# Kernel optimization log

Hardware: AMD Instinct MI355X
Metric: run time of the kernel (lower is better)

Reference implementation:

```python
import jax, jax.numpy as jnp
import numpy as np

DIM = 256
NUM_HEADS = 4
HEAD_DIM = DIM // NUM_HEADS


def _linear_params(k, d_in, d_out):
    kw, kb = jax.random.split(k)
    lim = 1.0 / np.sqrt(d_in)
    W = jax.random.uniform(kw, (d_out, d_in), jnp.float32, -lim, lim)
    b = jax.random.uniform(kb, (d_out,), jnp.float32, -lim, lim)
    return W, b


def setup_inputs() -> dict:
    key = jax.random.key(0)
    ks = jax.random.split(key, 10)
    B, Nq, Nkv = 8, 4096, 256
    inp = {
        'node_emb': jax.random.normal(ks[0], (B, Nq, DIM), jnp.float32),
        'cluster_emb': jax.random.normal(ks[1], (B, Nkv, DIM), jnp.float32),
        'clustering_weights': jax.random.normal(ks[2], (B, Nq, Nkv), jnp.float32),
        'ln_q_g': jnp.ones((DIM,), jnp.float32), 'ln_q_b': jnp.zeros((DIM,), jnp.float32),
        'ln_kv_g': jnp.ones((DIM,), jnp.float32), 'ln_kv_b': jnp.zeros((DIM,), jnp.float32),
        'ln_out_g': jnp.ones((DIM,), jnp.float32), 'ln_out_b': jnp.zeros((DIM,), jnp.float32),
    }
    for name, k in [('q', ks[3]), ('k', ks[4]), ('v', ks[5]), ('o', ks[6])]:
        W, b = _linear_params(k, DIM, DIM)
        inp[f'W_{name}'], inp[f'b_{name}'] = W, b
    W1, b1 = _linear_params(ks[7], DIM, DIM)
    W2, b2 = _linear_params(ks[8], DIM, DIM)
    inp.update(W_m1=W1, b_m1=b1, W_m2=W2, b_m2=b2)
    return inp


def _layer_norm(x, g, b, eps=1e-5):
    mu = jnp.mean(x, axis=-1, keepdims=True)
    var = jnp.var(x, axis=-1, keepdims=True)
    return (x - mu) * jax.lax.rsqrt(var + eps) * g + b


def reference(node_emb, cluster_emb, clustering_weights,
              ln_q_g, ln_q_b, ln_kv_g, ln_kv_b, ln_out_g, ln_out_b,
              W_q, b_q, W_k, b_k, W_v, b_v, W_o, b_o,
              W_m1, b_m1, W_m2, b_m2):
    B, Nq, D = node_emb.shape
    Nkv = cluster_emb.shape[1]
    q_in = _layer_norm(node_emb, ln_q_g, ln_q_b)
    kv_in = _layer_norm(cluster_emb, ln_kv_g, ln_kv_b)
    # projections -> [B, H, N, hd]
    Q = (q_in @ W_q.T + b_q).reshape(B, Nq, NUM_HEADS, HEAD_DIM).transpose(0, 2, 1, 3)
    K = (kv_in @ W_k.T + b_k).reshape(B, Nkv, NUM_HEADS, HEAD_DIM).transpose(0, 2, 1, 3)
    V = (kv_in @ W_v.T + b_v).reshape(B, Nkv, NUM_HEADS, HEAD_DIM).transpose(0, 2, 1, 3)
    scores = jnp.einsum('bhqd,bhkd->bhqk', Q, K) / np.sqrt(HEAD_DIM)
    scores = scores + clustering_weights[:, None, :, :]
    attn = jax.nn.softmax(scores, axis=-1)
    ctx = jnp.einsum('bhqk,bhkd->bhqd', attn, V)
    ctx = ctx.transpose(0, 2, 1, 3).reshape(B, Nq, D)
    attn_out = ctx @ W_o.T + b_o
    x = node_emb + attn_out
    h = _layer_norm(x, ln_out_g, ln_out_b)
    h = jax.nn.gelu(h @ W_m1.T + b_m1, approximate=False) @ W_m2.T + b_m2
    out = x + h
    attn_matrix = attn.mean(axis=1)
    return out, attn_matrix
```

## Files before the change

kernel.cpp:

```cpp
#include <hip/hip_runtime.h>
#include <math.h>

typedef __attribute__((ext_vector_type(8))) short short8;
typedef __attribute__((ext_vector_type(4))) float f32x4;
typedef __attribute__((ext_vector_type(2))) unsigned int u32x2;

#define AS1 __attribute__((address_space(1)))
#define AS3 __attribute__((address_space(3)))

__device__ __forceinline__ float b2f(short s){
  return __uint_as_float(((unsigned int)(unsigned short)s) << 16);
}
__device__ __forceinline__ short f2b(float f){
  unsigned int u = __float_as_uint(f);
  u = (u + 0x7fffu + ((u >> 16) & 1u)) >> 16;
  return (short)u;
}
__device__ __forceinline__ unsigned pk2(float lo, float hi){
  return ((unsigned)(unsigned short)f2b(hi) << 16) | (unsigned)(unsigned short)f2b(lo);
}
__device__ __forceinline__ float ulo(unsigned u){ return __uint_as_float(u << 16); }
__device__ __forceinline__ float uhi(unsigned u){ return __uint_as_float(u & 0xffff0000u); }

__global__ __launch_bounds__(256) void cvt_w(
    const float* __restrict__ s0, const float* __restrict__ s1,
    const float* __restrict__ s2, const float* __restrict__ s3,
    const float* __restrict__ s4, const float* __restrict__ s5,
    short* __restrict__ dst, short* __restrict__ dstS)
{
  const float* srcs[6] = {s0, s1, s2, s3, s4, s5};
  int i = blockIdx.x * 256 + threadIdx.x;
  int mat = i >> 16, rc = i & 65535;
  short v = f2b(srcs[mat][rc]);
  dst[i] = v;
  if (mat >= 3){
    int row = rc >> 8, col = rc & 255;
    int d2 = (mat - 3) * 65536 + ((col >> 5) << 13) + (row << 5)
           + (((col >> 3) & 3) << 3) + (col & 7);
    dstS[d2] = v;
  }
}

__global__ __launch_bounds__(256) void ln_k(
    const float* __restrict__ x, const float* __restrict__ g,
    const float* __restrict__ bta, short* __restrict__ y)
{
  const int row = blockIdx.x, t = threadIdx.x;
  const size_t base = (size_t)row * 256;
  float v = x[base + t];
  float s1 = v, s2 = v * v;
  #pragma unroll
  for (int off = 32; off; off >>= 1){ s1 += __shfl_down(s1, off); s2 += __shfl_down(s2, off); }
  __shared__ float a1[4], a2[4];
  __shared__ float mu_s, rs_s;
  if ((t & 63) == 0){ a1[t >> 6] = s1; a2[t >> 6] = s2; }
  __syncthreads();
  if (t == 0){
    float S1 = a1[0] + a1[1] + a1[2] + a1[3];
    float S2 = a2[0] + a2[1] + a2[2] + a2[3];
    float mu = S1 * 0.00390625f;
    float var = S2 * 0.00390625f - mu * mu;
    mu_s = mu; rs_s = rsqrtf(var + 1e-5f);
  }
  __syncthreads();
  y[base + t] = f2b((v - mu_s) * rs_s * g[t] + bta[t]);
}

template<int OT, int LNA>
__global__ __launch_bounds__(256, 2) void gemmW(
    const short* __restrict__ A, const float* __restrict__ Af,
    const short* __restrict__ W, const float* __restrict__ bias,
    short* __restrict__ outB,
    const float* __restrict__ lnag, const float* __restrict__ lnab)
{
  __shared__ short As[64][264];
  __shared__ short Ws[2][256][40];
  const int tid = threadIdx.x;
  const int m0 = blockIdx.x << 6;
  const int w = tid >> 6, lane = tid & 63;
  const int l15 = lane & 15, g = lane >> 4;

  if (LNA){
    const int row = tid >> 2, c0 = (tid & 3) << 6;
    float vv[64];
    const float* src = &Af[(size_t)(m0 + row) * 256 + c0];
    #pragma unroll
    for (int i = 0; i < 16; ++i) *(f32x4*)&vv[4 * i] = *(const f32x4*)&src[4 * i];
    float s1 = 0.f, s2 = 0.f;
    #pragma unroll
    for (int i = 0; i < 64; ++i){ s1 += vv[i]; s2 += vv[i] * vv[i]; }
    s1 += __shfl_xor(s1, 1); s2 += __shfl_xor(s2, 1);
    s1 += __shfl_xor(s1, 2); s2 += __shfl_xor(s2, 2);
    const float mu = s1 * 0.00390625f;
    const float rs = rsqrtf(s2 * 0.00390625f - mu * mu + 1e-5f);
    #pragma unroll
    for (int i = 0; i < 8; ++i){
      f32x4 gv0 = *(const f32x4*)&lnag[c0 + 8 * i];
      f32x4 gv1 = *(const f32x4*)&lnag[c0 + 8 * i + 4];
      f32x4 bv0 = *(const f32x4*)&lnab[c0 + 8 * i];
      f32x4 bv1 = *(const f32x4*)&lnab[c0 + 8 * i + 4];
      short8 o;
      #pragma unroll
      for (int j = 0; j < 4; ++j) o[j] = f2b((vv[8 * i + j] - mu) * rs * gv0[j] + bv0[j]);
      #pragma unroll
      for (int j = 0; j < 4; ++j) o[4 + j] = f2b((vv[8 * i + 4 + j] - mu) * rs * gv1[j] + bv1[j]);
      *(short8*)&As[row][c0 + 8 * i] = o;
    }
  } else {
    #pragma unroll
    for (int it = 0; it < 8; ++it){
      int idx = tid + (it << 8);
      int row = idx >> 5, c = (idx & 31) << 3;
      *(short8*)&As[row][c] = *(const short8*)&A[(size_t)(m0 + row) * 256 + c];
    }
  }
  #pragma unroll
  for (int it = 0; it < 4; ++it){
    int row = (it << 6) + (tid >> 2), c = (tid & 3) << 3;
    *(short8*)&Ws[0][row][c] = *(const short8*)&W[(size_t)row * 256 + c];
  }
  __syncthreads();

  f32x4 acc[16];
  #pragma unroll
  for (int nt = 0; nt < 16; ++nt) acc[nt] = {0.f, 0.f, 0.f, 0.f};

  int cur = 0;
  for (int s = 0; s < 8; ++s){
    const int k0 = s << 5;
    short8 wreg[4];
    if (s < 7){
      #pragma unroll
      for (int it = 0; it < 4; ++it)
        wreg[it] = *(const short8*)&W[(size_t)((it << 6) + (tid >> 2)) * 256 + k0 + 32 + ((tid & 3) << 3)];
    }
    short8 af = *(const short8*)&As[(w << 4) + l15][k0 + (g << 3)];
    #pragma unroll
    for (int nt = 0; nt < 16; ++nt){
      short8 bf = *(const short8*)&Ws[cur][(nt << 4) + l15][g << 3];
      acc[nt] = __builtin_amdgcn_mfma_f32_16x16x32_bf16(af, bf, acc[nt], 0, 0, 0);
    }
    if (s < 7){
      #pragma unroll
      for (int it = 0; it < 4; ++it)
        *(short8*)&Ws[cur ^ 1][(it << 6) + (tid >> 2)][(tid & 3) << 3] = wreg[it];
    }
    __syncthreads();
    cur ^= 1;
  }

  const int row_l = (w << 4) + (g << 2);
  #pragma unroll
  for (int nt = 0; nt < 16; ++nt){
    const int col = (nt << 4) + l15;
    const float bv = bias[col];
    #pragma unroll
    for (int r = 0; r < 4; ++r){
      const int m = m0 + row_l + r;
      float v = acc[nt][r] + bv;
      if (OT == 1){
        const int b_ = m >> 8, kvr = m & 255;
        const int knt = kvr >> 4, kl = kvr & 15;
        const int h = col >> 6, half = (col >> 5) & 1, kg = (col >> 3) & 3, kj = col & 7;
        outB[(((((size_t)(b_ * 4 + h) * 16 + knt) * 2 + half) * 4 + kg) * 16 + kl) * 8 + kj] = f2b(v);
      }
      if (OT == 2){
        const int b_ = m >> 8, kvj = m & 255;
        const int jp = (kvj & ~31) | (((kvj >> 2) & 3) << 3) | (((kvj >> 4) & 1) << 2) | (kvj & 3);
        const int h = col >> 6, dp = col & 63;
        const int kk = jp >> 5, vg = (jp >> 3) & 3, vj = jp & 7;
        const int vn2 = dp >> 4, vl = dp & 15;
        outB[(((((size_t)(b_ * 4 + h) * 8 + kk) * 4 + vn2) * 4 + vg) * 16 + vl) * 8 + vj] = f2b(v);
      }
      if (OT == 4){
        outB[((((size_t)blockIdx.x * 8 + (col >> 5)) * 4 + w) * 64
              + (((col >> 3) & 3) << 4) + (g << 2) + r) * 8 + (col & 7)] = f2b(v);
      }
    }
  }
}

__global__ __launch_bounds__(256, 2) void attn_k(
    const short* __restrict__ Qf, const short* __restrict__ Kf,
    const short* __restrict__ Vf, const float* __restrict__ cw,
    short* __restrict__ ctx, float* __restrict__ am_out)
{
  extern __shared__ __align__(16) short smem[];
  short* Kl = smem;
  short* Vl = smem + 16384;
  const int b = blockIdx.y;
  const int q0 = blockIdx.x << 6;
  const int tid = threadIdx.x;
  const int w = tid >> 6, lane = tid & 63;
  const int l15 = lane & 15, g = lane >> 4;
  const size_t qw = (size_t)b * 4096 + q0 + (w << 4);
  const size_t qblk = qw >> 4;
  const size_t tileQ = qblk >> 2;
  const int wQ = (int)(qblk & 3);
  const size_t tileC = (size_t)b * 64 + blockIdx.x;

#define STG(dst_, src_) do{ _Pragma("unroll")                                        \
  for (int it_ = 0; it_ < 8; ++it_){ int c_ = (it_ << 8) + tid;                      \
    __builtin_amdgcn_global_load_lds((const AS1 void*)((src_) + (c_ << 3)),          \
                                     (AS3 void*)((dst_) + (c_ << 3)), 16, 0, 0); } }while(0)

  unsigned cwp[16][2];
  f32x4 am[16];
  {
    char* reg = (char*)smem + (w << 13);
    #pragma unroll
    for (int j = 0; j < 16; ++j){
      f32x4 v = *(const f32x4*)&cw[(qw + j) * 256 + (lane << 2)];
      u32x2 d = { pk2(v[0], v[1]), pk2(v[2], v[3]) };
      unsigned off = ((j << 9) + (lane << 3)) ^ ((j & 7) << 4);
      *(u32x2*)(reg + off) = d;
    }
    __syncthreads();
    #pragma unroll
    for (int nt = 0; nt < 16; ++nt){
      unsigned base = ((l15 << 9) + (nt << 5) + (g << 3)) ^ ((l15 & 7) << 4);
      cwp[nt][0] = *(const unsigned*)(reg + base);
      cwp[nt][1] = *(const unsigned*)(reg + base + 4);
      am[nt] = {0.f, 0.f, 0.f, 0.f};
    }
    __syncthreads();
  }

  STG(Kl, Kf + ((size_t)(b * 4) << 14));
  __syncthreads();

  for (int h = 0; h < 4; ++h){
    STG(Vl, Vf + ((size_t)(b * 4 + h) << 14));
    short8 qf0 = *(const short8*)&Qf[(((tileQ * 8 + (h << 1)) * 4 + wQ) * 64 + lane) * 8];
    short8 qf1 = *(const short8*)&Qf[(((tileQ * 8 + (h << 1) + 1) * 4 + wQ) * 64 + lane) * 8];

    f32x4 acc[16];
    #pragma unroll
    for (int nt = 0; nt < 16; ++nt) acc[nt] = {0.f, 0.f, 0.f, 0.f};
    #pragma unroll
    for (int nt = 0; nt < 16; ++nt){
      short8 kf0 = *(const short8*)&Kl[(nt << 10) + (lane << 3)];
      acc[nt] = __builtin_amdgcn_mfma_f32_16x16x32_bf16(kf0, qf0, acc[nt], 0, 0, 0);
      short8 kf1 = *(const short8*)&Kl[(nt << 10) + 512 + (lane << 3)];
      acc[nt] = __builtin_amdgcn_mfma_f32_16x16x32_bf16(kf1, qf1, acc[nt], 0, 0, 0);
    }
    __syncthreads();
    if (h < 3) STG(Kl, Kf + ((size_t)(b * 4 + h + 1) << 14));

    float mx = -3.4e38f;
    #pragma unroll
    for (int nt = 0; nt < 16; ++nt){
      float c0 = __uint_as_float(cwp[nt][0] << 16);
      float c1 = __uint_as_float(cwp[nt][0] & 0xffff0000u);
      float c2 = __uint_as_float(cwp[nt][1] << 16);
      float c3 = __uint_as_float(cwp[nt][1] & 0xffff0000u);
      acc[nt][0] = acc[nt][0] * 0.125f + c0;
      acc[nt][1] = acc[nt][1] * 0.125f + c1;
      acc[nt][2] = acc[nt][2] * 0.125f + c2;
      acc[nt][3] = acc[nt][3] * 0.125f + c3;
      mx = fmaxf(mx, fmaxf(fmaxf(acc[nt][0], acc[nt][1]), fmaxf(acc[nt][2], acc[nt][3])));
    }
    mx = fmaxf(mx, __shfl_xor(mx, 16));
    mx = fmaxf(mx, __shfl_xor(mx, 32));
    float sm = 0.f;
    #pragma unroll
    for (int nt = 0; nt < 16; ++nt){
      #pragma unroll
      for (int r = 0; r < 4; ++r){
        float e = __expf(acc[nt][r] - mx);
        acc[nt][r] = e; sm += e;
      }
    }
    sm += __shfl_xor(sm, 16);
    sm += __shfl_xor(sm, 32);
    float inv = 1.f / sm;
    #pragma unroll
    for (int nt = 0; nt < 16; ++nt){
      #pragma unroll
      for (int r = 0; r < 4; ++r){
        float p = acc[nt][r] * inv;
        acc[nt][r] = p;
        am[nt][r] += 0.25f * p;
      }
    }
    f32x4 oc[4] = {{0,0,0,0},{0,0,0,0},{0,0,0,0},{0,0,0,0}};
    #pragma unroll
    for (int kk = 0; kk < 8; ++kk){
      union { short8 s; unsigned u[4]; } pa;
      pa.u[0] = pk2(acc[2 * kk][0],     acc[2 * kk][1]);
      pa.u[1] = pk2(acc[2 * kk][2],     acc[2 * kk][3]);
      pa.u[2] = pk2(acc[2 * kk + 1][0], acc[2 * kk + 1][1]);
      pa.u[3] = pk2(acc[2 * kk + 1][2], acc[2 * kk + 1][3]);
      #pragma unroll
      for (int n2 = 0; n2 < 4; ++n2){
        short8 vb = *(const short8*)&Vl[(((kk << 2) + n2) << 9) + (lane << 3)];
        oc[n2] = __builtin_amdgcn_mfma_f32_16x16x32_bf16(pa.s, vb, oc[n2], 0, 0, 0);
      }
    }
    #pragma unroll
    for (int n2 = 0; n2 < 4; ++n2){
      const int sctx = (h << 1) + (n2 >> 1);
      const int gctx = ((n2 & 1) << 1) + (l15 >> 3);
      const int j = l15 & 7;
      #pragma unroll
      for (int r = 0; r < 4; ++r)
        ctx[(((tileC * 8 + sctx) * 4 + w) * 64 + (gctx << 4) + (g << 2) + r) * 8 + j]
            = f2b(oc[n2][r]);
    }
    __syncthreads();
  }

  {
    char* reg = (char*)smem + (w << 14);
    #pragma unroll
    for (int nt = 0; nt < 16; ++nt){
      unsigned off = ((l15 << 10) + (nt << 6) + (g << 4)) ^ ((l15 & 7) << 4);
      *(f32x4*)(reg + off) = am[nt];
    }
    __syncthreads();
    #pragma unroll
    for (int i2 = 0; i2 < 16; ++i2){
      unsigned fb = (tid << 4) + (i2 << 12);
      unsigned rowin = (fb >> 10) & 15;
      f32x4 v = *(const f32x4*)((char*)smem + (fb ^ ((rowin & 7) << 4)));
      unsigned row = fb >> 10;
      *(f32x4*)&am_out[((size_t)b * 4096 + q0 + row) * 256 + ((fb & 1023) >> 2)] = v;
    }
  }
#undef STG
}

__global__ __launch_bounds__(256, 2) void tail_k(
    const short* __restrict__ ctxaf, const short* __restrict__ Wst,
    const float* __restrict__ b_o, const float* __restrict__ b_m1,
    const float* __restrict__ b_m2, const float* __restrict__ node,
    const float* __restrict__ lng, const float* __restrict__ lnb,
    float* __restrict__ outF)
{
  extern __shared__ __align__(16) short lds[];
  short* Ws0 = lds + 16896;
  short* Ws1 = Ws0 + 8192;
  const int tid = threadIdx.x;
  const int tile = blockIdx.x;
  const int m0 = tile << 6;
  const int w = tid >> 6, lane = tid & 63;
  const int l15 = lane & 15, g = lane >> 4;
  const int row_l = (w << 4) + (g << 2);

#define ASW(row_, col_) (*(short*)((char*)lds + (row_) * 528 + \
    (((col_) ^ ((((row_) >> 2) & 3) << 3)) << 1)))
#define ASR8(row_, boff_) (*(const short8*)((char*)lds + (row_) * 528 + \
    ((boff_) ^ ((((row_) >> 2) & 3) << 4))))
#define STGW(dst_, wmat_, s_) do{ _Pragma("unroll")                                  \
  for (int it_ = 0; it_ < 4; ++it_){ int c_ = (it_ << 8) + tid;                      \
    __builtin_amdgcn_global_load_lds(                                               \
        (const AS1 void*)((wmat_) + ((size_t)(s_) << 13) + (c_ << 3)),              \
        (AS3 void*)((dst_) + (c_ << 3)), 16, 0, 0); } }while(0)
#define KLOOP(WMAT, AF_EXPR)                                                         \
  do{ int cur = 0;                                                                   \
    _Pragma("unroll")                                                                \
    for (int s = 0; s < 8; ++s){                                                     \
      short* rbuf = cur ? Ws1 : Ws0;                                                 \
      short* sbuf = cur ? Ws0 : Ws1;                                                 \
      if (s < 7){ STGW(sbuf, WMAT, s + 1);                                           \
        asm volatile("s_waitcnt vmcnt(4)" ::: "memory");                             \
      } else {                                                                       \
        asm volatile("s_waitcnt vmcnt(0)" ::: "memory");                             \
      }                                                                              \
      __builtin_amdgcn_s_barrier();                                                  \
      const short8 af = (AF_EXPR);                                                   \
      _Pragma("unroll")                                                              \
      for (int nt = 0; nt < 16; ++nt){                                               \
        short8 bf = *(const short8*)&rbuf[((nt << 4) + l15) * 32 + (g << 3)];        \
        acc[nt] = __builtin_amdgcn_mfma_f32_16x16x32_bf16(af, bf, acc[nt], 0, 0, 0); \
      }                                                                              \
      __builtin_amdgcn_s_barrier();                                                  \
      cur ^= 1;                                                                      \
    } }while(0)

  f32x4 acc[16];

  STGW(Ws0, Wst, 0);
  short8 afr[8];
  #pragma unroll
  for (int s = 0; s < 8; ++s)
    afr[s] = *(const short8*)&ctxaf[((((size_t)tile << 3) + s) * 4 + w) * 512 + (lane << 3)];
  #pragma unroll
  for (int nt = 0; nt < 16; ++nt) acc[nt] = {0.f, 0.f, 0.f, 0.f};
  KLOOP(Wst, afr[s]);

  unsigned xvp[16][2];
  #pragma unroll
  for (int nt = 0; nt < 16; ++nt){
    const int col = (nt << 4) + l15;
    const float bv = b_o[col];
    float x0 = acc[nt][0] + bv + node[(size_t)(m0 + row_l + 0) * 256 + col];
    float x1 = acc[nt][1] + bv + node[(size_t)(m0 + row_l + 1) * 256 + col];
    float x2 = acc[nt][2] + bv + node[(size_t)(m0 + row_l + 2) * 256 + col];
    float x3 = acc[nt][3] + bv + node[(size_t)(m0 + row_l + 3) * 256 + col];
    xvp[nt][0] = pk2(x0, x1);
    xvp[nt][1] = pk2(x2, x3);
  }
  #pragma unroll
  for (int r = 0; r < 4; ++r){
    float s1 = 0.f, s2 = 0.f;
    #pragma unroll
    for (int nt = 0; nt < 16; ++nt){
      float v = (r == 0) ? ulo(xvp[nt][0]) : (r == 1) ? uhi(xvp[nt][0])
              : (r == 2) ? ulo(xvp[nt][1]) : uhi(xvp[nt][1]);
      s1 += v; s2 += v * v;
    }
    #pragma unroll
    for (int off = 1; off < 16; off <<= 1){ s1 += __shfl_xor(s1, off); s2 += __shfl_xor(s2, off); }
    const float mu = s1 * 0.00390625f;
    const float rs = rsqrtf(s2 * 0.00390625f - mu * mu + 1e-5f);
    #pragma unroll
    for (int nt = 0; nt < 16; ++nt){
      const int col = (nt << 4) + l15;
      float v = (r == 0) ? ulo(xvp[nt][0]) : (r == 1) ? uhi(xvp[nt][0])
              : (r == 2) ? ulo(xvp[nt][1]) : uhi(xvp[nt][1]);
      ASW(row_l + r, col) = f2b((v - mu) * rs * lng[col] + lnb[col]);
    }
  }

  {
    const short* Wm1 = Wst + 65536;
    STGW(Ws0, Wm1, 0);
    __syncthreads();
    #pragma unroll
    for (int nt = 0; nt < 16; ++nt) acc[nt] = {0.f, 0.f, 0.f, 0.f};
    KLOOP(Wm1, ASR8((w << 4) + l15, (s << 6) + (g << 4)));
  }
  #pragma unroll
  for (int nt = 0; nt < 16; ++nt){
    const int col = (nt << 4) + l15;
    const float bv = b_m1[col];
    #pragma unroll
    for (int r = 0; r < 4; ++r){
      float v = acc[nt][r] + bv;
      v = 0.5f * v * (1.0f + erff(v * 0.70710678118f));
      ASW(row_l + r, col) = f2b(v);
    }
  }

  {
    const short* Wm2 = Wst + 131072;
    STGW(Ws0, Wm2, 0);
    __syncthreads();
    #pragma unroll
    for (int nt = 0; nt < 16; ++nt) acc[nt] = {0.f, 0.f, 0.f, 0.f};
    KLOOP(Wm2, ASR8((w << 4) + l15, (s << 6) + (g << 4)));
  }
  #pragma unroll
  for (int nt = 0; nt < 16; ++nt){
    const int col = (nt << 4) + l15;
    const float bv = b_m2[col];
    #pragma unroll
    for (int r = 0; r < 4; ++r){
      float xr = (r == 0) ? ulo(xvp[nt][0]) : (r == 1) ? uhi(xvp[nt][0])
               : (r == 2) ? ulo(xvp[nt][1]) : uhi(xvp[nt][1]);
      outF[(size_t)(m0 + row_l + r) * 256 + col] = acc[nt][r] + bv + xr;
    }
  }
#undef ASW
#undef ASR8
#undef STGW
#undef KLOOP
}

extern "C" void kernel_launch(void* const* d_in, const int* in_sizes, int n_in,
                              void* d_out, int out_size, void* d_ws, size_t ws_size,
                              hipStream_t stream)
{
  const float* node_emb = (const float*)d_in[0];
  const float* cluster  = (const float*)d_in[1];
  const float* cw       = (const float*)d_in[2];
  const float* ln_q_g   = (const float*)d_in[3];
  const float* ln_q_b   = (const float*)d_in[4];
  const float* ln_kv_g  = (const float*)d_in[5];
  const float* ln_kv_b  = (const float*)d_in[6];
  const float* ln_o_g   = (const float*)d_in[7];
  const float* ln_o_b   = (const float*)d_in[8];
  const float* W_q  = (const float*)d_in[9];  const float* b_q  = (const float*)d_in[10];
  const float* W_k  = (const float*)d_in[11]; const float* b_k  = (const float*)d_in[12];
  const float* W_v  = (const float*)d_in[13]; const float* b_v  = (const float*)d_in[14];
  const float* W_o  = (const float*)d_in[15]; const float* b_o  = (const float*)d_in[16];
  const float* W_m1 = (const float*)d_in[17]; const float* b_m1 = (const float*)d_in[18];
  const float* W_m2 = (const float*)d_in[19]; const float* b_m2 = (const float*)d_in[20];

  char* ws = (char*)d_ws;
  short* Wbf   = (short*)ws;
  short* Wst   = (short*)(ws + 786432);
  short* bufA  = (short*)(ws + 1179648);
  short* bufB  = (short*)(ws + 1179648 + 16777216);
  short* kvin  = (short*)(ws + 1179648 + 2 * 16777216);
  short* kfrag = (short*)(ws + 1179648 + 2 * 16777216 + 1048576);
  short* vfrag = (short*)(ws + 1179648 + 2 * 16777216 + 2 * 1048576);

  float* outF = (float*)d_out;
  float* amof = (float*)d_out + 8388608;

  hipFuncSetAttribute((const void*)attn_k, hipFuncAttributeMaxDynamicSharedMemorySize, 65536);
  hipFuncSetAttribute((const void*)tail_k, hipFuncAttributeMaxDynamicSharedMemorySize, 66560);

  cvt_w<<<1536, 256, 0, stream>>>(W_q, W_k, W_v, W_o, W_m1, W_m2, Wbf, Wst);
  ln_k<<<2048, 256, 0, stream>>>(cluster, ln_kv_g, ln_kv_b, kvin);
  gemmW<4,1><<<512, 256, 0, stream>>>(nullptr, node_emb, Wbf, b_q, bufB, ln_q_g, ln_q_b);
  gemmW<1,0><<<32, 256, 0, stream>>>(kvin, nullptr, Wbf + 65536,  b_k, kfrag, nullptr, nullptr);
  gemmW<2,0><<<32, 256, 0, stream>>>(kvin, nullptr, Wbf + 131072, b_v, vfrag, nullptr, nullptr);
  attn_k<<<dim3(64, 8), 256, 65536, stream>>>(bufB, kfrag, vfrag, cw, bufA, amof);
  tail_k<<<512, 256, 66560, stream>>>(bufA, Wst, b_o, b_m1, b_m2,
      node_emb, ln_o_g, ln_o_b, outF);
}
```

Before: 121.9 us.

## Fuse KV layernorm into K/V projections and halve tail weight stage buffers

Drops the separate layer-norm kernel for cluster embeddings. The K and V projection GEMMs now apply layer norm on the fly from fp32 input using their existing LNA path. Separately, the tail kernel streams weight tiles in half-sized chunks (16 steps instead of 8), which cuts dynamic LDS from 66560 to 50176 bytes so more blocks may fit per CU. The cost is twice as many barriers and waits per GEMM in the tail, and the layer norm is now computed twice, once in each projection kernel.

```diff
diff --git a/kernel.cpp b/kernel.cpp
--- a/kernel.cpp
+++ b/kernel.cpp
@@ -39,31 +39,6 @@
            + (((col >> 3) & 3) << 3) + (col & 7);
     dstS[d2] = v;
   }
-}
-
-__global__ __launch_bounds__(256) void ln_k(
-    const float* __restrict__ x, const float* __restrict__ g,
-    const float* __restrict__ bta, short* __restrict__ y)
-{
-  const int row = blockIdx.x, t = threadIdx.x;
-  const size_t base = (size_t)row * 256;
-  float v = x[base + t];
-  float s1 = v, s2 = v * v;
-  #pragma unroll
-  for (int off = 32; off; off >>= 1){ s1 += __shfl_down(s1, off); s2 += __shfl_down(s2, off); }
-  __shared__ float a1[4], a2[4];
-  __shared__ float mu_s, rs_s;
-  if ((t & 63) == 0){ a1[t >> 6] = s1; a2[t >> 6] = s2; }
-  __syncthreads();
-  if (t == 0){
-    float S1 = a1[0] + a1[1] + a1[2] + a1[3];
-    float S2 = a2[0] + a2[1] + a2[2] + a2[3];
-    float mu = S1 * 0.00390625f;
-    float var = S2 * 0.00390625f - mu * mu;
-    mu_s = mu; rs_s = rsqrtf(var + 1e-5f);
-  }
-  __syncthreads();
-  y[base + t] = f2b((v - mu_s) * rs_s * g[t] + bta[t]);
 }
 
 template<int OT, int LNA>
@@ -339,7 +314,7 @@
 {
   extern __shared__ __align__(16) short lds[];
   short* Ws0 = lds + 16896;
-  short* Ws1 = Ws0 + 8192;
+  short* Ws1 = Ws0 + 4096;
   const int tid = threadIdx.x;
   const int tile = blockIdx.x;
   const int m0 = tile << 6;
@@ -351,36 +326,42 @@
     (((col_) ^ ((((row_) >> 2) & 3) << 3)) << 1)))
 #define ASR8(row_, boff_) (*(const short8*)((char*)lds + (row_) * 528 + \
     ((boff_) ^ ((((row_) >> 2) & 3) << 4))))
-#define STGW(dst_, wmat_, s_) do{ _Pragma("unroll")                                  \
-  for (int it_ = 0; it_ < 4; ++it_){ int c_ = (it_ << 8) + tid;                      \
+#define STGH(dst_, wmat_, t_) do{ _Pragma("unroll")                                  \
+  for (int it_ = 0; it_ < 2; ++it_){ int c_ = (it_ << 8) + tid;                      \
     __builtin_amdgcn_global_load_lds(                                               \
-        (const AS1 void*)((wmat_) + ((size_t)(s_) << 13) + (c_ << 3)),              \
+        (const AS1 void*)((wmat_) + ((size_t)(t_) << 12) + (c_ << 3)),              \
         (AS3 void*)((dst_) + (c_ << 3)), 16, 0, 0); } }while(0)
 #define KLOOP(WMAT, AF_EXPR)                                                         \
   do{ int cur = 0;                                                                   \
+    short8 af;                                                                       \
     _Pragma("unroll")                                                                \
     for (int s = 0; s < 8; ++s){                                                     \
-      short* rbuf = cur ? Ws1 : Ws0;                                                 \
-      short* sbuf = cur ? Ws0 : Ws1;                                                 \
-      if (s < 7){ STGW(sbuf, WMAT, s + 1);                                           \
-        asm volatile("s_waitcnt vmcnt(4)" ::: "memory");                             \
-      } else {                                                                       \
-        asm volatile("s_waitcnt vmcnt(0)" ::: "memory");                             \
+      _Pragma("unroll")                                                              \
+      for (int half = 0; half < 2; ++half){                                          \
+        const int t = (s << 1) + half;                                               \
+        short* rbuf = cur ? Ws1 : Ws0;                                               \
+        short* sbuf = cur ? Ws0 : Ws1;                                               \
+        if (t < 15){ STGH(sbuf, WMAT, t + 1);                                        \
+          asm volatile("s_waitcnt vmcnt(2)" ::: "memory");                           \
+        } else {                                                                     \
+          asm volatile("s_waitcnt vmcnt(0)" ::: "memory");                           \
+        }                                                                            \
+        __builtin_amdgcn_s_barrier();                                                \
+        if (half == 0) af = (AF_EXPR);                                               \
+        _Pragma("unroll")                                                            \
+        for (int ntl = 0; ntl < 8; ++ntl){                                           \
+          short8 bf = *(const short8*)&rbuf[((ntl << 4) + l15) * 32 + (g << 3)];     \
+          acc[(half << 3) + ntl] =                                                   \
+              __builtin_amdgcn_mfma_f32_16x16x32_bf16(af, bf, acc[(half << 3) + ntl], 0, 0, 0); \
+        }                                                                            \
+        __builtin_amdgcn_s_barrier();                                                \
+        cur ^= 1;                                                                    \
       }                                                                              \
-      __builtin_amdgcn_s_barrier();                                                  \
-      const short8 af = (AF_EXPR);                                                   \
-      _Pragma("unroll")                                                              \
-      for (int nt = 0; nt < 16; ++nt){                                               \
-        short8 bf = *(const short8*)&rbuf[((nt << 4) + l15) * 32 + (g << 3)];        \
-        acc[nt] = __builtin_amdgcn_mfma_f32_16x16x32_bf16(af, bf, acc[nt], 0, 0, 0); \
-      }                                                                              \
-      __builtin_amdgcn_s_barrier();                                                  \
-      cur ^= 1;                                                                      \
     } }while(0)
 
   f32x4 acc[16];
 
-  STGW(Ws0, Wst, 0);
+  STGH(Ws0, Wst, 0);
   short8 afr[8];
   #pragma unroll
   for (int s = 0; s < 8; ++s)
@@ -425,7 +406,7 @@
 
   {
     const short* Wm1 = Wst + 65536;
-    STGW(Ws0, Wm1, 0);
+    STGH(Ws0, Wm1, 0);
     __syncthreads();
     #pragma unroll
     for (int nt = 0; nt < 16; ++nt) acc[nt] = {0.f, 0.f, 0.f, 0.f};
@@ -445,7 +426,7 @@
 
   {
     const short* Wm2 = Wst + 131072;
-    STGW(Ws0, Wm2, 0);
+    STGH(Ws0, Wm2, 0);
     __syncthreads();
     #pragma unroll
     for (int nt = 0; nt < 16; ++nt) acc[nt] = {0.f, 0.f, 0.f, 0.f};
@@ -464,7 +445,7 @@
   }
 #undef ASW
 #undef ASR8
-#undef STGW
+#undef STGH
 #undef KLOOP
 }
 
@@ -493,7 +474,6 @@
   short* Wst   = (short*)(ws + 786432);
   short* bufA  = (short*)(ws + 1179648);
   short* bufB  = (short*)(ws + 1179648 + 16777216);
-  short* kvin  = (short*)(ws + 1179648 + 2 * 16777216);
   short* kfrag = (short*)(ws + 1179648 + 2 * 16777216 + 1048576);
   short* vfrag = (short*)(ws + 1179648 + 2 * 16777216 + 2 * 1048576);
 
@@ -501,14 +481,13 @@
   float* amof = (float*)d_out + 8388608;
 
   hipFuncSetAttribute((const void*)attn_k, hipFuncAttributeMaxDynamicSharedMemorySize, 65536);
-  hipFuncSetAttribute((const void*)tail_k, hipFuncAttributeMaxDynamicSharedMemorySize, 66560);
+  hipFuncSetAttribute((const void*)tail_k, hipFuncAttributeMaxDynamicSharedMemorySize, 50176);
 
   cvt_w<<<1536, 256, 0, stream>>>(W_q, W_k, W_v, W_o, W_m1, W_m2, Wbf, Wst);
-  ln_k<<<2048, 256, 0, stream>>>(cluster, ln_kv_g, ln_kv_b, kvin);
   gemmW<4,1><<<512, 256, 0, stream>>>(nullptr, node_emb, Wbf, b_q, bufB, ln_q_g, ln_q_b);
-  gemmW<1,0><<<32, 256, 0, stream>>>(kvin, nullptr, Wbf + 65536,  b_k, kfrag, nullptr, nullptr);
-  gemmW<2,0><<<32, 256, 0, stream>>>(kvin, nullptr, Wbf + 131072, b_v, vfrag, nullptr, nullptr);
+  gemmW<1,1><<<32, 256, 0, stream>>>(nullptr, cluster, Wbf + 65536,  b_k, kfrag, ln_kv_g, ln_kv_b);
+  gemmW<2,1><<<32, 256, 0, stream>>>(nullptr, cluster, Wbf + 131072, b_v, vfrag, ln_kv_g, ln_kv_b);
   attn_k<<<dim3(64, 8), 256, 65536, stream>>>(bufB, kfrag, vfrag, cw, bufA, amof);
-  tail_k<<<512, 256, 66560, stream>>>(bufA, Wst, b_o, b_m1, b_m2,
+  tail_k<<<512, 256, 50176, stream>>>(bufA, Wst, b_o, b_m1, b_m2,
       node_emb, ln_o_g, ln_o_b, outF);
 }
```

Result: slower. 128.6 us (+5.5%).

## Split tail kernel N dimension across two waves per row block with 512 threads

Applied to the files above, without the earlier changes.

The fused output-projection/LayerNorm/MLP tail kernel now runs 8 waves per block instead of 4. Each pair of waves shares a 16-row slab and splits the 256 output columns in half, so per-wave accumulators drop from 16 to 8 tiles. This lowers register pressure and raises the number of waves available to hide latency. LayerNorm statistics are now combined across the two column halves through a small LDS partial-sum buffer plus an extra block barrier, and sched_barriers are added around the k-loop barriers. The launch bound of 4 blocks of 512 threads per CU is unlikely to be met given the roughly 66 KB of LDS per block.

```diff
diff --git a/kernel.cpp b/kernel.cpp
--- a/kernel.cpp
+++ b/kernel.cpp
@@ -330,7 +330,7 @@
 #undef STG
 }
 
-__global__ __launch_bounds__(256, 2) void tail_k(
+__global__ __launch_bounds__(512, 4) void tail_k(
     const short* __restrict__ ctxaf, const short* __restrict__ Wst,
     const float* __restrict__ b_o, const float* __restrict__ b_m1,
     const float* __restrict__ b_m2, const float* __restrict__ node,
@@ -340,19 +340,22 @@
   extern __shared__ __align__(16) short lds[];
   short* Ws0 = lds + 16896;
   short* Ws1 = Ws0 + 8192;
+  float* part = (float*)(lds + 33280);
   const int tid = threadIdx.x;
   const int tile = blockIdx.x;
   const int m0 = tile << 6;
   const int w = tid >> 6, lane = tid & 63;
   const int l15 = lane & 15, g = lane >> 4;
-  const int row_l = (w << 4) + (g << 2);
+  const int wm = w >> 1, wn = w & 1;
+  const int row_l = (wm << 4) + (g << 2);
+  const int colb = wn << 7;
 
 #define ASW(row_, col_) (*(short*)((char*)lds + (row_) * 528 + \
     (((col_) ^ ((((row_) >> 2) & 3) << 3)) << 1)))
 #define ASR8(row_, boff_) (*(const short8*)((char*)lds + (row_) * 528 + \
     ((boff_) ^ ((((row_) >> 2) & 3) << 4))))
 #define STGW(dst_, wmat_, s_) do{ _Pragma("unroll")                                  \
-  for (int it_ = 0; it_ < 4; ++it_){ int c_ = (it_ << 8) + tid;                      \
+  for (int it_ = 0; it_ < 2; ++it_){ int c_ = (it_ << 9) + tid;                      \
     __builtin_amdgcn_global_load_lds(                                               \
         (const AS1 void*)((wmat_) + ((size_t)(s_) << 13) + (c_ << 3)),              \
         (AS3 void*)((dst_) + (c_ << 3)), 16, 0, 0); } }while(0)
@@ -363,63 +366,76 @@
       short* rbuf = cur ? Ws1 : Ws0;                                                 \
       short* sbuf = cur ? Ws0 : Ws1;                                                 \
       if (s < 7){ STGW(sbuf, WMAT, s + 1);                                           \
-        asm volatile("s_waitcnt vmcnt(4)" ::: "memory");                             \
+        asm volatile("s_waitcnt vmcnt(2)" ::: "memory");                             \
       } else {                                                                       \
         asm volatile("s_waitcnt vmcnt(0)" ::: "memory");                             \
       }                                                                              \
       __builtin_amdgcn_s_barrier();                                                  \
+      __builtin_amdgcn_sched_barrier(0);                                             \
       const short8 af = (AF_EXPR);                                                   \
       _Pragma("unroll")                                                              \
-      for (int nt = 0; nt < 16; ++nt){                                               \
-        short8 bf = *(const short8*)&rbuf[((nt << 4) + l15) * 32 + (g << 3)];        \
-        acc[nt] = __builtin_amdgcn_mfma_f32_16x16x32_bf16(af, bf, acc[nt], 0, 0, 0); \
+      for (int ntl = 0; ntl < 8; ++ntl){                                             \
+        short8 bf = *(const short8*)&rbuf[(((wn << 3) + ntl) * 16 + l15) * 32 + (g << 3)]; \
+        acc[ntl] = __builtin_amdgcn_mfma_f32_16x16x32_bf16(af, bf, acc[ntl], 0, 0, 0); \
       }                                                                              \
       __builtin_amdgcn_s_barrier();                                                  \
+      __builtin_amdgcn_sched_barrier(0);                                             \
       cur ^= 1;                                                                      \
     } }while(0)
 
-  f32x4 acc[16];
+  f32x4 acc[8];
 
   STGW(Ws0, Wst, 0);
   short8 afr[8];
   #pragma unroll
   for (int s = 0; s < 8; ++s)
-    afr[s] = *(const short8*)&ctxaf[((((size_t)tile << 3) + s) * 4 + w) * 512 + (lane << 3)];
-  #pragma unroll
-  for (int nt = 0; nt < 16; ++nt) acc[nt] = {0.f, 0.f, 0.f, 0.f};
+    afr[s] = *(const short8*)&ctxaf[((((size_t)tile << 3) + s) * 4 + wm) * 512 + (lane << 3)];
+  #pragma unroll
+  for (int ntl = 0; ntl < 8; ++ntl) acc[ntl] = {0.f, 0.f, 0.f, 0.f};
   KLOOP(Wst, afr[s]);
 
-  unsigned xvp[16][2];
-  #pragma unroll
-  for (int nt = 0; nt < 16; ++nt){
-    const int col = (nt << 4) + l15;
+  unsigned xvp[8][2];
+  #pragma unroll
+  for (int ntl = 0; ntl < 8; ++ntl){
+    const int col = colb + (ntl << 4) + l15;
     const float bv = b_o[col];
-    float x0 = acc[nt][0] + bv + node[(size_t)(m0 + row_l + 0) * 256 + col];
-    float x1 = acc[nt][1] + bv + node[(size_t)(m0 + row_l + 1) * 256 + col];
-    float x2 = acc[nt][2] + bv + node[(size_t)(m0 + row_l + 2) * 256 + col];
-    float x3 = acc[nt][3] + bv + node[(size_t)(m0 + row_l + 3) * 256 + col];
-    xvp[nt][0] = pk2(x0, x1);
-    xvp[nt][1] = pk2(x2, x3);
+    float x0 = acc[ntl][0] + bv + node[(size_t)(m0 + row_l + 0) * 256 + col];
+    float x1 = acc[ntl][1] + bv + node[(size_t)(m0 + row_l + 1) * 256 + col];
+    float x2 = acc[ntl][2] + bv + node[(size_t)(m0 + row_l + 2) * 256 + col];
+    float x3 = acc[ntl][3] + bv + node[(size_t)(m0 + row_l + 3) * 256 + col];
+    xvp[ntl][0] = pk2(x0, x1);
+    xvp[ntl][1] = pk2(x2, x3);
   }
   #pragma unroll
   for (int r = 0; r < 4; ++r){
     float s1 = 0.f, s2 = 0.f;
     #pragma unroll
-    for (int nt = 0; nt < 16; ++nt){
-      float v = (r == 0) ? ulo(xvp[nt][0]) : (r == 1) ? uhi(xvp[nt][0])
-              : (r == 2) ? ulo(xvp[nt][1]) : uhi(xvp[nt][1]);
+    for (int ntl = 0; ntl < 8; ++ntl){
+      float v = (r == 0) ? ulo(xvp[ntl][0]) : (r == 1) ? uhi(xvp[ntl][0])
+              : (r == 2) ? ulo(xvp[ntl][1]) : uhi(xvp[ntl][1]);
       s1 += v; s2 += v * v;
     }
     #pragma unroll
     for (int off = 1; off < 16; off <<= 1){ s1 += __shfl_xor(s1, off); s2 += __shfl_xor(s2, off); }
-    const float mu = s1 * 0.00390625f;
-    const float rs = rsqrtf(s2 * 0.00390625f - mu * mu + 1e-5f);
-    #pragma unroll
-    for (int nt = 0; nt < 16; ++nt){
-      const int col = (nt << 4) + l15;
-      float v = (r == 0) ? ulo(xvp[nt][0]) : (r == 1) ? uhi(xvp[nt][0])
-              : (r == 2) ? ulo(xvp[nt][1]) : uhi(xvp[nt][1]);
-      ASW(row_l + r, col) = f2b((v - mu) * rs * lng[col] + lnb[col]);
+    if (l15 == 0){
+      part[((row_l + r) * 2 + wn) * 2]     = s1;
+      part[((row_l + r) * 2 + wn) * 2 + 1] = s2;
+    }
+  }
+  __syncthreads();
+  #pragma unroll
+  for (int r = 0; r < 4; ++r){
+    const int row = row_l + r;
+    const float S1 = part[(row * 2) * 2]     + part[(row * 2 + 1) * 2];
+    const float S2 = part[(row * 2) * 2 + 1] + part[(row * 2 + 1) * 2 + 1];
+    const float mu = S1 * 0.00390625f;
+    const float rs = rsqrtf(S2 * 0.00390625f - mu * mu + 1e-5f);
+    #pragma unroll
+    for (int ntl = 0; ntl < 8; ++ntl){
+      const int col = colb + (ntl << 4) + l15;
+      float v = (r == 0) ? ulo(xvp[ntl][0]) : (r == 1) ? uhi(xvp[ntl][0])
+              : (r == 2) ? ulo(xvp[ntl][1]) : uhi(xvp[ntl][1]);
+      ASW(row, col) = f2b((v - mu) * rs * lng[col] + lnb[col]);
     }
   }
 
@@ -428,16 +444,16 @@
     STGW(Ws0, Wm1, 0);
     __syncthreads();
     #pragma unroll
-    for (int nt = 0; nt < 16; ++nt) acc[nt] = {0.f, 0.f, 0.f, 0.f};
-    KLOOP(Wm1, ASR8((w << 4) + l15, (s << 6) + (g << 4)));
-  }
-  #pragma unroll
-  for (int nt = 0; nt < 16; ++nt){
-    const int col = (nt << 4) + l15;
+    for (int ntl = 0; ntl < 8; ++ntl) acc[ntl] = {0.f, 0.f, 0.f, 0.f};
+    KLOOP(Wm1, ASR8((wm << 4) + l15, (s << 6) + (g << 4)));
+  }
+  #pragma unroll
+  for (int ntl = 0; ntl < 8; ++ntl){
+    const int col = colb + (ntl << 4) + l15;
     const float bv = b_m1[col];
     #pragma unroll
     for (int r = 0; r < 4; ++r){
-      float v = acc[nt][r] + bv;
+      float v = acc[ntl][r] + bv;
       v = 0.5f * v * (1.0f + erff(v * 0.70710678118f));
       ASW(row_l + r, col) = f2b(v);
     }
@@ -448,18 +464,18 @@
     STGW(Ws0, Wm2, 0);
     __syncthreads();
     #pragma unroll
-    for (int nt = 0; nt < 16; ++nt) acc[nt] = {0.f, 0.f, 0.f, 0.f};
-    KLOOP(Wm2, ASR8((w << 4) + l15, (s << 6) + (g << 4)));
-  }
-  #pragma unroll
-  for (int nt = 0; nt < 16; ++nt){
-    const int col = (nt << 4) + l15;
+    for (int ntl = 0; ntl < 8; ++ntl) acc[ntl] = {0.f, 0.f, 0.f, 0.f};
+    KLOOP(Wm2, ASR8((wm << 4) + l15, (s << 6) + (g << 4)));
+  }
+  #pragma unroll
+  for (int ntl = 0; ntl < 8; ++ntl){
+    const int col = colb + (ntl << 4) + l15;
     const float bv = b_m2[col];
     #pragma unroll
     for (int r = 0; r < 4; ++r){
-      float xr = (r == 0) ? ulo(xvp[nt][0]) : (r == 1) ? uhi(xvp[nt][0])
-               : (r == 2) ? ulo(xvp[nt][1]) : uhi(xvp[nt][1]);
-      outF[(size_t)(m0 + row_l + r) * 256 + col] = acc[nt][r] + bv + xr;
+      float xr = (r == 0) ? ulo(xvp[ntl][0]) : (r == 1) ? uhi(xvp[ntl][0])
+               : (r == 2) ? ulo(xvp[ntl][1]) : uhi(xvp[ntl][1]);
+      outF[(size_t)(m0 + row_l + r) * 256 + col] = acc[ntl][r] + bv + xr;
     }
   }
 #undef ASW
@@ -501,7 +517,7 @@
   float* amof = (float*)d_out + 8388608;
 
   hipFuncSetAttribute((const void*)attn_k, hipFuncAttributeMaxDynamicSharedMemorySize, 65536);
-  hipFuncSetAttribute((const void*)tail_k, hipFuncAttributeMaxDynamicSharedMemorySize, 66560);
+  hipFuncSetAttribute((const void*)tail_k, hipFuncAttributeMaxDynamicSharedMemorySize, 67584);
 
   cvt_w<<<1536, 256, 0, stream>>>(W_q, W_k, W_v, W_o, W_m1, W_m2, Wbf, Wst);
   ln_k<<<2048, 256, 0, stream>>>(cluster, ln_kv_g, ln_kv_b, kvin);
@@ -509,6 +525,6 @@
   gemmW<1,0><<<32, 256, 0, stream>>>(kvin, nullptr, Wbf + 65536,  b_k, kfrag, nullptr, nullptr);
   gemmW<2,0><<<32, 256, 0, stream>>>(kvin, nullptr, Wbf + 131072, b_v, vfrag, nullptr, nullptr);
   attn_k<<<dim3(64, 8), 256, 65536, stream>>>(bufB, kfrag, vfrag, cw, bufA, amof);
-  tail_k<<<512, 256, 66560, stream>>>(bufA, Wst, b_o, b_m1, b_m2,
+  tail_k<<<512, 512, 67584, stream>>>(bufA, Wst, b_o, b_m1, b_m2,
       node_emb, ln_o_g, ln_o_b, outF);
 }
```

Measured after the change: 119.4 us. 2.0% less time.
